# Kernel optimization log

Hardware: AMD Instinct MI355X
Metric: run time of the kernel (lower is better)

The kernel has to match this reference:

```python
import jax, jax.numpy as jnp
import numpy as np

N = 100000      # nodes
E = 1600000     # edges
R = 8           # relation types
D = 128         # in_dim = h_dim = out_dim

def setup_inputs() -> dict:
    key = jax.random.key(0)
    ks = jax.random.split(key, 10)
    feats = jax.random.normal(ks[0], (N, D), dtype=jnp.float32)
    src = jax.random.randint(ks[1], (E,), 0, N, dtype=jnp.int32)
    dst = jax.random.randint(ks[2], (E,), 0, N, dtype=jnp.int32)
    etype = jax.random.randint(ks[3], (E,), 0, R, dtype=jnp.int32)
    s = 0.05  # keep activations well-scaled
    W1 = jax.random.normal(ks[4], (R, D, D), dtype=jnp.float32) * s
    loop_w1 = jax.random.normal(ks[5], (D, D), dtype=jnp.float32) * s
    b1 = jnp.zeros((D,), dtype=jnp.float32)
    W2 = jax.random.normal(ks[6], (R, D, D), dtype=jnp.float32) * s
    loop_w2 = jax.random.normal(ks[7], (D, D), dtype=jnp.float32) * s
    b2 = jnp.zeros((D,), dtype=jnp.float32)
    return {"feats": feats, "W1": W1, "loop_w1": loop_w1, "b1": b1,
            "W2": W2, "loop_w2": loop_w2, "b2": b2,
            "src": src, "dst": dst, "etype": etype}

def _rel_conv(h, W, loop_w, b, src, dst, etype, relu):
    # Per-relation transform of all node features: [R, N, out]
    # (cheaper than gathering a per-edge [E, in, out] weight tensor)
    h_rel = jnp.einsum('ni,rio->rno', h, W)
    # Per-edge message = W_{etype(e)} @ h[src(e)] : [E, out]
    msg = h_rel[etype, src]
    # Sum-aggregate messages at destination nodes
    agg = jax.ops.segment_sum(msg, dst, num_segments=h.shape[0])
    out = agg + h @ loop_w + b  # self-loop + bias
    return jax.nn.relu(out) if relu else out

def reference(feats, W1, loop_w1, b1, W2, loop_w2, b2, src, dst, etype):
    # eval-mode forward: dropout is identity
    h = _rel_conv(feats, W1, loop_w1, b1, src, dst, etype, relu=True)
    h = _rel_conv(h, W2, loop_w2, b2, src, dst, etype, relu=False)
    return h
```

## Files before the change

kernel.cpp:

```cpp
#include <hip/hip_runtime.h>
#include <hip/hip_bf16.h>


#define D 128
#define KTOT 1152
#define KACC 1024
#define BK 32
#define BSH 9
#define BSZ 512
#define TILE 4096

typedef __attribute__((ext_vector_type(8))) __bf16 bf16x8;
typedef __attribute__((ext_vector_type(8))) unsigned short us8;
typedef __attribute__((ext_vector_type(4))) unsigned short us4;
typedef __attribute__((ext_vector_type(4))) float f32x4;

__device__ __forceinline__ unsigned short f2bf(float f) {
    union { float f; unsigned u; } v; v.f = f;
    unsigned r = v.u + 0x7FFF + ((v.u >> 16) & 1);
    return (unsigned short)(r >> 16);
}
__device__ __forceinline__ float bf2f(unsigned short u) {
    return __uint_as_float((unsigned)u << 16);
}

__device__ __forceinline__ int lds_off(int row, int c) {
    return row * 32 + ((c ^ ((row >> 1) & 3)) << 3);
}


__global__ __launch_bounds__(256) void histA_kernel(const int* __restrict__ dst,
                                                    int* __restrict__ bcnt, int E, int nbuck) {
    __shared__ int c[1024];
    int t = threadIdx.x;
    for (int i = t; i < nbuck; i += 256) c[i] = 0;
    __syncthreads();
    int stride = gridDim.x * 256;
    for (int e = blockIdx.x * 256 + t; e < E; e += stride)
        atomicAdd(&c[dst[e] >> BSH], 1);
    __syncthreads();
    for (int i = t; i < nbuck; i += 256)
        if (c[i]) atomicAdd(&bcnt[i], c[i]);
}

__global__ __launch_bounds__(1024) void scanA_kernel(const int* __restrict__ bcnt,
                                                     int* __restrict__ boffs,
                                                     int* __restrict__ bhead, int nbuck) {
    int t = threadIdx.x;
    int v = (t < nbuck) ? bcnt[t] : 0;
    int lane = t & 63, w = t >> 6;
    int inc = v;
    #pragma unroll
    for (int off = 1; off < 64; off <<= 1) {
        int n = __shfl_up(inc, off, 64);
        if (lane >= off) inc += n;
    }
    __shared__ int ws[16];
    if (lane == 63) ws[w] = inc;
    __syncthreads();
    int wbase = 0;
    for (int i = 0; i < w; ++i) wbase += ws[i];
    int ex = wbase + inc - v;
    if (t < nbuck) { boffs[t] = ex; bhead[t] = ex; }
    if (t == nbuck - 1) boffs[nbuck] = ex + v;
}

__global__ __launch_bounds__(1024) void scatterA_kernel(const int* __restrict__ src,
                                                        const int* __restrict__ dst,
                                                        const int* __restrict__ et,
                                                        int* __restrict__ bhead,
                                                        int* __restrict__ sortedA, int E, int nbuck) {
    __shared__ int skey[TILE];
    __shared__ unsigned char sbkt[TILE];
    __shared__ int cnt[256];
    __shared__ int lpos[256];
    __shared__ int gdelta[256];
    __shared__ int ws[4];
    const int t = threadIdx.x;
    const int e0 = blockIdx.x * TILE;
    int dreg[4];

    if (t < 256) cnt[t] = 0;
    __syncthreads();
    #pragma unroll
    for (int j = 0; j < 4; ++j) {
        int e = e0 + j * 1024 + t;
        int d = -1;
        if (e < E) { d = dst[e]; atomicAdd(&cnt[d >> BSH], 1); }
        dreg[j] = d;
    }
    __syncthreads();
    int c = 0, inc = 0;
    const int lane = t & 63, w = t >> 6;
    if (t < 256) {
        c = cnt[t];
        inc = c;
        #pragma unroll
        for (int off = 1; off < 64; off <<= 1) {
            int n = __shfl_up(inc, off, 64);
            if (lane >= off) inc += n;
        }
        if (lane == 63) ws[w] = inc;
    }
    __syncthreads();
    if (t < 256) {
        int wbase = 0;
        for (int i = 0; i < w; ++i) wbase += ws[i];
        int ex = wbase + inc - c;
        lpos[t] = ex;
        if (c) gdelta[t] = atomicAdd(&bhead[t], c) - ex;
    }
    __syncthreads();
    #pragma unroll
    for (int j = 0; j < 4; ++j) {
        int e = e0 + j * 1024 + t;
        if (e < E) {
            int d = dreg[j];
            int b = d >> BSH;
            int key = ((d & (BSZ - 1)) << 20) | (et[e] << 17) | src[e];
            int p = atomicAdd(&lpos[b], 1);
            skey[p] = key;
            sbkt[p] = (unsigned char)b;
        }
    }
    __syncthreads();
    int ntile = min(TILE, E - e0);
    for (int i = t; i < ntile; i += 1024)
        sortedA[gdelta[sbkt[i]] + i] = skey[i];
}


__global__ __launch_bounds__(512) void passB_kernel(const int* __restrict__ sortedA,
                                                    const int* __restrict__ boffs,
                                                    int* __restrict__ sorted,
                                                    int* __restrict__ offs2,
                                                    int N8, int E, int nbuck) {
    __shared__ int cnt[4096];
    __shared__ int cur[4096];
    __shared__ int ws[8];
    const int b = blockIdx.x;
    const int t = threadIdx.x;
    const int gb0 = boffs[b], gb1 = boffs[b + 1];
    #pragma unroll
    for (int i = 0; i < 8; ++i) cnt[i * 512 + t] = 0;
    __syncthreads();
    for (int e = gb0 + t; e < gb1; e += 512) {
        int k = sortedA[e];
        atomicAdd(&cnt[(k >> 17) & 4095], 1);
    }
    __syncthreads();
    const int base = t * 8;
    int s = 0;
    #pragma unroll
    for (int i = 0; i < 8; ++i) s += cnt[base + i];
    int lane = t & 63, w = t >> 6;
    int inc = s;
    #pragma unroll
    for (int off = 1; off < 64; off <<= 1) {
        int n = __shfl_up(inc, off, 64);
        if (lane >= off) inc += n;
    }
    if (lane == 63) ws[w] = inc;
    __syncthreads();
    int wbase = 0;
    for (int i = 0; i < w; ++i) wbase += ws[i];
    int run = gb0 + wbase + inc - s;
    int g0 = (b << 12) + base;
    #pragma unroll
    for (int i = 0; i < 8; ++i) {
        int cv = cnt[base + i];
        cur[base + i] = run;
        if (g0 + i <= N8) offs2[g0 + i] = run;
        run += cv;
    }
    __syncthreads();
    for (int e = gb0 + t; e < gb1; e += 512) {
        int k = sortedA[e];
        int p = atomicAdd(&cur[(k >> 17) & 4095], 1);
        sorted[p] = k;
    }
}


__global__ void cast_kernel(const float* __restrict__ W1, const float* __restrict__ lw1,
                            const float* __restrict__ W2, const float* __restrict__ lw2,
                            const float* __restrict__ feats,
                            unsigned short* __restrict__ Bt1, unsigned short* __restrict__ Bt2,
                            unsigned short* __restrict__ hb0, int n4) {
    const int per = KTOT * D;
    int idx = blockIdx.x * blockDim.x + threadIdx.x;
    if (idx < 2 * per) {
        int layer = idx / per;
        int rem = idx - layer * per;
        int k = rem >> 7;
        int o = rem & 127;
        const float* W  = layer ? W2 : W1;
        const float* lw = layer ? lw2 : lw1;
        float val = (k < 1024) ? W[k * D + o] : lw[(k - 1024) * D + o];
        unsigned short* Bt = layer ? Bt2 : Bt1;
        Bt[o * KTOT + k] = f2bf(val);
    } else {
        int i = idx - 2 * per;
        if (i < n4) {
            float4 v = *(const float4*)(feats + (size_t)i * 4);
            us4 o; o.x = f2bf(v.x); o.y = f2bf(v.y); o.z = f2bf(v.z); o.w = f2bf(v.w);
            *(us4*)(hb0 + (size_t)i * 4) = o;
        }
    }
}


__global__ __launch_bounds__(256) void aggregate_kernel(const unsigned short* __restrict__ hb,
                                                        const int* __restrict__ offs2,
                                                        const int* __restrict__ sorted,
                                                        unsigned short* __restrict__ A,
                                                        int v0, int vend) {
    const int t = threadIdx.x;
    const int c = (t & 15) * 8;
    const int gu = blockIdx.x * 16 + (t >> 4);
    const int v = v0 + (gu >> 3);
    const int r = gu & 7;
    if (v >= vend) return;

    const int e0 = offs2[v * 8 + r];
    const int e1 = offs2[v * 8 + r + 1];

    float a0[8], a1[8];
    #pragma unroll
    for (int j = 0; j < 8; ++j) { a0[j] = 0.f; a1[j] = 0.f; }

    int e = e0;
    for (; e + 1 < e1; e += 2) {
        int p0 = sorted[e], p1 = sorted[e + 1];
        us8 h0 = *(const us8*)(hb + (size_t)(p0 & 131071) * D + c);
        us8 h1 = *(const us8*)(hb + (size_t)(p1 & 131071) * D + c);
        #pragma unroll
        for (int j = 0; j < 8; ++j) { a0[j] += bf2f(h0[j]); a1[j] += bf2f(h1[j]); }
    }
    if (e < e1) {
        int p0 = sorted[e];
        us8 h0 = *(const us8*)(hb + (size_t)(p0 & 131071) * D + c);
        #pragma unroll
        for (int j = 0; j < 8; ++j) a0[j] += bf2f(h0[j]);
    }

    us8 o;
    #pragma unroll
    for (int j = 0; j < 8; ++j) o[j] = f2bf(a0[j] + a1[j]);
    *(us8*)(A + (size_t)(v - v0) * KACC + r * 128 + c) = o;
}


__global__ __launch_bounds__(256) void gemm_kernel(const unsigned short* __restrict__ A,
                                                   const unsigned short* __restrict__ hbA,
                                                   const unsigned short* __restrict__ Bt,
                                                   const float* __restrict__ bias,
                                                   float* __restrict__ outf,
                                                   unsigned short* __restrict__ outb,
                                                   int v0, int vend, int relu_bf) {
    __shared__ unsigned short Alds[64 * 32];
    __shared__ unsigned short Blds[128 * 32];
    const int t = threadIdx.x;
    const int lane = t & 63;
    const int w = t >> 6;
    const int quad = lane >> 4;
    const int c16 = lane & 15;
    const int blockRow0 = v0 + blockIdx.x * 64;

    const int srow = t >> 2;
    const int schunk = t & 3;

    f32x4 acc[8];
    #pragma unroll
    for (int j = 0; j < 8; ++j) acc[j] = f32x4{0.f, 0.f, 0.f, 0.f};

    const int aRow = blockRow0 + srow;
    const bool aval = aRow < vend;
    const us8 zz = {0, 0, 0, 0, 0, 0, 0, 0};
    const unsigned short* Arow = A + (size_t)(aRow - v0) * KACC + schunk * 8;
    const unsigned short* Hrow = hbA + (size_t)aRow * D + schunk * 8;
    const unsigned short* Brow0 = Bt + (size_t)srow * KTOT + schunk * 8;
    const unsigned short* Brow1 = Bt + (size_t)(srow + 64) * KTOT + schunk * 8;

    us8 av = zz;
    if (aval) av = *(const us8*)(Arow);
    us8 bv0 = *(const us8*)(Brow0);
    us8 bv1 = *(const us8*)(Brow1);

    for (int k0 = 0; k0 < KTOT; k0 += BK) {
        us8 na = zz, nb0 = zz, nb1 = zz;
        const int kn = k0 + BK;
        if (kn < KTOT) {
            if (aval) {
                if (kn < KACC) na = *(const us8*)(Arow + kn);
                else           na = *(const us8*)(Hrow + (kn - KACC));
            }
            nb0 = *(const us8*)(Brow0 + kn);
            nb1 = *(const us8*)(Brow1 + kn);
        }
        __syncthreads();
        *(us8*)(Alds + lds_off(srow, schunk)) = av;
        *(us8*)(Blds + lds_off(srow,      schunk)) = bv0;
        *(us8*)(Blds + lds_off(srow + 64, schunk)) = bv1;
        __syncthreads();

        bf16x8 af = *(const bf16x8*)(Alds + lds_off(w * 16 + c16, quad));
        #pragma unroll
        for (int ct = 0; ct < 8; ++ct) {
            bf16x8 bfr = *(const bf16x8*)(Blds + lds_off(ct * 16 + c16, quad));
            acc[ct] = __builtin_amdgcn_mfma_f32_16x16x32_bf16(af, bfr, acc[ct], 0, 0, 0);
        }
        av = na; bv0 = nb0; bv1 = nb1;
    }

    int row = blockRow0 + w * 16 + quad * 4;
    #pragma unroll
    for (int ct = 0; ct < 8; ++ct) {
        int col = ct * 16 + c16;
        float bcol = bias[col];
        #pragma unroll
        for (int i = 0; i < 4; ++i) {
            int r = row + i;
            if (r < vend) {
                float vv = acc[ct][i] + bcol;
                if (relu_bf) {
                    vv = fmaxf(vv, 0.f);
                    outb[(size_t)r * D + col] = f2bf(vv);
                } else {
                    outf[(size_t)r * D + col] = vv;
                }
            }
        }
    }
}


extern "C" void kernel_launch(void* const* d_in, const int* in_sizes, int n_in,
                              void* d_out, int out_size, void* d_ws, size_t ws_size,
                              hipStream_t stream) {
    const float* feats = (const float*)d_in[0];
    const float* W1    = (const float*)d_in[1];
    const float* lw1   = (const float*)d_in[2];
    const float* b1    = (const float*)d_in[3];
    const float* W2    = (const float*)d_in[4];
    const float* lw2   = (const float*)d_in[5];
    const float* b2    = (const float*)d_in[6];
    const int*   src   = (const int*)d_in[7];
    const int*   dst   = (const int*)d_in[8];
    const int*   etype = (const int*)d_in[9];
    const int N = in_sizes[0] / D;
    const int E = in_sizes[7];
    float* out = (float*)d_out;

    const int nbuck = (N + BSZ - 1) >> BSH;

    size_t woff = 0;
    auto take = [&](size_t bytes) -> void* {
        void* p = (char*)d_ws + woff;
        woff += (bytes + 255) & ~(size_t)255;
        return p;
    };
    unsigned short* ACC = (unsigned short*)take((size_t)N * KACC * 2);
    int* sortedA        = (int*)ACC;
    int* bcnt           = (int*)((char*)ACC + (((size_t)E * 4 + 255) & ~(size_t)255));
    int* boffs          = bcnt + 1024;
    int* bhead          = boffs + 1032;
    int* offs2          = (int*)take((size_t)(N * 8 + 1) * 4);
    int* sorted         = (int*)take((size_t)E * 4);
    unsigned short* Bt1 = (unsigned short*)take((size_t)KTOT * D * 2);
    unsigned short* Bt2 = (unsigned short*)take((size_t)KTOT * D * 2);
    unsigned short* hb0 = (unsigned short*)take((size_t)N * D * 2);
    unsigned short* hb1 = (unsigned short*)take((size_t)N * D * 2);

    (void)hipMemsetAsync(bcnt, 0, (size_t)nbuck * 4, stream);

    histA_kernel<<<1024, 256, 0, stream>>>(dst, bcnt, E, nbuck);
    scanA_kernel<<<1, 1024, 0, stream>>>(bcnt, boffs, bhead, nbuck);
    scatterA_kernel<<<(E + TILE - 1) / TILE, 1024, 0, stream>>>(src, dst, etype, bhead, sortedA, E, nbuck);
    passB_kernel<<<nbuck, 512, 0, stream>>>(sortedA, boffs, sorted, offs2, N * 8, E, nbuck);

    int n4 = N * D / 4;
    int cb = (2 * KTOT * D + n4 + 255) / 256;
    cast_kernel<<<cb, 256, 0, stream>>>(W1, lw1, W2, lw2, feats, Bt1, Bt2, hb0, n4);

    int ab = (N * 8 + 15) / 16;
    int gb = (N + 63) / 64;
    for (int layer = 0; layer < 2; ++layer) {
        const unsigned short* hin = layer ? hb1 : hb0;
        const unsigned short* Bt  = layer ? Bt2 : Bt1;
        const float* bias         = layer ? b2  : b1;
        aggregate_kernel<<<ab, 256, 0, stream>>>(hin, offs2, sorted, ACC, 0, N);
        gemm_kernel<<<gb, 256, 0, stream>>>(ACC, hin, Bt, bias, out, hb1, 0, N, 1 - layer);
    }
}
```

Measured before the change: 506.0 us.

## Overlap half-graph GEMM with aggregation of the other half in a joint kernel

Splits the nodes into two halves per layer. The first half is aggregated first. A combined kernel then runs the GEMM on that half while other blocks aggregate the second half, and a final GEMM covers the second half. The aim is to overlap the compute-bound GEMM with the gather-bound aggregation and cut idle time at kernel boundaries. The cost is one extra launch per layer. The joint kernel's register and LDS footprint is the larger of the two bodies, which may lower occupancy for its aggregation blocks.

```diff
diff --git a/kernel.cpp b/kernel.cpp
--- a/kernel.cpp
+++ b/kernel.cpp
@@ -210,14 +210,15 @@
 }
 
 
-__global__ __launch_bounds__(256) void aggregate_kernel(const unsigned short* __restrict__ hb,
-                                                        const int* __restrict__ offs2,
-                                                        const int* __restrict__ sorted,
-                                                        unsigned short* __restrict__ A,
-                                                        int v0, int vend) {
+__device__ __forceinline__ void aggregate_body(int blk,
+                                               const unsigned short* __restrict__ hb,
+                                               const int* __restrict__ offs2,
+                                               const int* __restrict__ sorted,
+                                               unsigned short* __restrict__ A,
+                                               int v0, int vend) {
     const int t = threadIdx.x;
     const int c = (t & 15) * 8;
-    const int gu = blockIdx.x * 16 + (t >> 4);
+    const int gu = blk * 16 + (t >> 4);
     const int v = v0 + (gu >> 3);
     const int r = gu & 7;
     if (v >= vend) return;
@@ -247,25 +248,24 @@
     us8 o;
     #pragma unroll
     for (int j = 0; j < 8; ++j) o[j] = f2bf(a0[j] + a1[j]);
-    *(us8*)(A + (size_t)(v - v0) * KACC + r * 128 + c) = o;
-}
-
-
-__global__ __launch_bounds__(256) void gemm_kernel(const unsigned short* __restrict__ A,
-                                                   const unsigned short* __restrict__ hbA,
-                                                   const unsigned short* __restrict__ Bt,
-                                                   const float* __restrict__ bias,
-                                                   float* __restrict__ outf,
-                                                   unsigned short* __restrict__ outb,
-                                                   int v0, int vend, int relu_bf) {
-    __shared__ unsigned short Alds[64 * 32];
-    __shared__ unsigned short Blds[128 * 32];
+    *(us8*)(A + (size_t)v * KACC + r * 128 + c) = o;
+}
+
+__device__ __forceinline__ void gemm_body(int blk,
+                                          const unsigned short* __restrict__ A,
+                                          const unsigned short* __restrict__ hbA,
+                                          const unsigned short* __restrict__ Bt,
+                                          const float* __restrict__ bias,
+                                          float* __restrict__ outf,
+                                          unsigned short* __restrict__ outb,
+                                          int v0, int vend, int relu_bf,
+                                          unsigned short* Alds, unsigned short* Blds) {
     const int t = threadIdx.x;
     const int lane = t & 63;
     const int w = t >> 6;
     const int quad = lane >> 4;
     const int c16 = lane & 15;
-    const int blockRow0 = v0 + blockIdx.x * 64;
+    const int blockRow0 = v0 + blk * 64;
 
     const int srow = t >> 2;
     const int schunk = t & 3;
@@ -277,7 +277,7 @@
     const int aRow = blockRow0 + srow;
     const bool aval = aRow < vend;
     const us8 zz = {0, 0, 0, 0, 0, 0, 0, 0};
-    const unsigned short* Arow = A + (size_t)(aRow - v0) * KACC + schunk * 8;
+    const unsigned short* Arow = A + (size_t)aRow * KACC + schunk * 8;
     const unsigned short* Hrow = hbA + (size_t)aRow * D + schunk * 8;
     const unsigned short* Brow0 = Bt + (size_t)srow * KTOT + schunk * 8;
     const unsigned short* Brow1 = Bt + (size_t)(srow + 64) * KTOT + schunk * 8;
@@ -331,6 +331,47 @@
                 }
             }
         }
+    }
+}
+
+
+__global__ __launch_bounds__(256) void aggregate_kernel(const unsigned short* __restrict__ hb,
+                                                        const int* __restrict__ offs2,
+                                                        const int* __restrict__ sorted,
+                                                        unsigned short* __restrict__ A,
+                                                        int v0, int vend) {
+    aggregate_body(blockIdx.x, hb, offs2, sorted, A, v0, vend);
+}
+
+__global__ __launch_bounds__(256) void gemm_kernel(const unsigned short* __restrict__ A,
+                                                   const unsigned short* __restrict__ hbA,
+                                                   const unsigned short* __restrict__ Bt,
+                                                   const float* __restrict__ bias,
+                                                   float* __restrict__ outf,
+                                                   unsigned short* __restrict__ outb,
+                                                   int v0, int vend, int relu_bf) {
+    __shared__ unsigned short Alds[64 * 32];
+    __shared__ unsigned short Blds[128 * 32];
+    gemm_body(blockIdx.x, A, hbA, Bt, bias, outf, outb, v0, vend, relu_bf, Alds, Blds);
+}
+
+__global__ __launch_bounds__(256) void joint_kernel(const unsigned short* __restrict__ ACC,
+                                                    const unsigned short* __restrict__ hin,
+                                                    const unsigned short* __restrict__ Bt,
+                                                    const float* __restrict__ bias,
+                                                    float* __restrict__ outf,
+                                                    unsigned short* __restrict__ outb,
+                                                    int gv0, int gvend, int relu_bf, int gb,
+                                                    const int* __restrict__ offs2,
+                                                    const int* __restrict__ sorted,
+                                                    unsigned short* __restrict__ ACCw,
+                                                    int av0, int avend) {
+    __shared__ unsigned short Alds[64 * 32];
+    __shared__ unsigned short Blds[128 * 32];
+    if ((int)blockIdx.x < gb) {
+        gemm_body(blockIdx.x, ACC, hin, Bt, bias, outf, outb, gv0, gvend, relu_bf, Alds, Blds);
+    } else {
+        aggregate_body(blockIdx.x - gb, hin, offs2, sorted, ACCw, av0, avend);
     }
 }
 
@@ -383,13 +424,22 @@
     int cb = (2 * KTOT * D + n4 + 255) / 256;
     cast_kernel<<<cb, 256, 0, stream>>>(W1, lw1, W2, lw2, feats, Bt1, Bt2, hb0, n4);
 
-    int ab = (N * 8 + 15) / 16;
-    int gb = (N + 63) / 64;
+    const int ch = (((N + 1) / 2) + 63) & ~63;
+    const int len1 = N - ch;
+    const int ab0 = (ch * 8 + 15) / 16;
+    const int ab1 = (len1 * 8 + 15) / 16;
+    const int gb0 = (ch + 63) / 64;
+    const int gb1 = (len1 + 63) / 64;
+
     for (int layer = 0; layer < 2; ++layer) {
         const unsigned short* hin = layer ? hb1 : hb0;
         const unsigned short* Bt  = layer ? Bt2 : Bt1;
         const float* bias         = layer ? b2  : b1;
-        aggregate_kernel<<<ab, 256, 0, stream>>>(hin, offs2, sorted, ACC, 0, N);
-        gemm_kernel<<<gb, 256, 0, stream>>>(ACC, hin, Bt, bias, out, hb1, 0, N, 1 - layer);
-    }
-}
+        const int relu            = 1 - layer;
+        aggregate_kernel<<<ab0, 256, 0, stream>>>(hin, offs2, sorted, ACC, 0, ch);
+        joint_kernel<<<gb0 + ab1, 256, 0, stream>>>(ACC, hin, Bt, bias, out, hb1,
+                                                    0, ch, relu, gb0,
+                                                    offs2, sorted, ACC, ch, N);
+        gemm_kernel<<<gb1, 256, 0, stream>>>(ACC, hin, Bt, bias, out, hb1, ch, N, relu);
+    }
+}
```

After: 536.3 us. +6.0%, slower.
